# Kernel optimization log

Measured on AMD Instinct MI355X. Metric: run time of the kernel, lower is better.

Reference implementation:

```python
import jax, jax.numpy as jnp
import numpy as np

N = 8192      # source grid points
M = 8192      # output grid points
NB = 16       # n_basis
WIDTH = 32    # int(n_basis * enhancement)
EPS = 1e-4
LOG2 = 0.6931471805599453


def log_cosh(x):
    a = jnp.abs(x)
    return a + jnp.log1p(jnp.exp(-2.0 * a)) - LOG2


def setup_inputs() -> dict:
    key = jax.random.key(0)
    ks = jax.random.split(key, 9)
    rho = jax.random.uniform(ks[0], (N,), minval=0.05, maxval=2.0)
    gamma = jax.random.uniform(ks[1], (N,), minval=0.01, maxval=1.0)
    coords = jax.random.normal(ks[2], (N, 3)) * 5.0
    weights = jax.random.uniform(ks[3], (N,), minval=0.0, maxval=0.1)
    out_coords = jax.random.normal(ks[4], (M, 3)) * 5.0
    # field_embed params: Linear(1 -> WIDTH), Linear(WIDTH -> NB)
    w1 = jax.random.normal(ks[5], (1, WIDTH)) * 1.0
    b1 = jax.random.normal(ks[6], (WIDTH,)) * 0.1
    w2 = jax.random.normal(ks[7], (WIDTH, NB)) / np.sqrt(WIDTH)
    b2 = jax.random.normal(ks[8], (NB,)) * 0.1
    return {"rho": rho, "gamma": gamma, "coords": coords, "weights": weights,
            "out_coords": out_coords, "w1": w1, "b1": b1, "w2": w2, "b2": b2}


def _field_embed(x, w1, b1, w2, b2):
    # x: (..., 1) -> (..., NB)
    return jnp.tanh(x @ w1 + b1) @ w2 + b2


def reference(rho, gamma, coords, weights, out_coords, w1, b1, w2, b2):
    # rescaled (reduced) density gradient s^2 = gamma / (4 (3 pi^2)^{2/3} rho^{8/3})
    s2 = gamma / (4.0 * (3.0 * jnp.pi ** 2) ** (2.0 / 3.0) * rho ** (8.0 / 3.0))
    x = jnp.log(s2 + EPS)[:, None]                     # (N, 1)
    exponent = log_cosh(_field_embed(x, w1, b1, w2, b2))  # (N, NB)
    heg_scale = log_cosh(_field_embed(jnp.zeros((1, 1), rho.dtype), w1, b1, w2, b2)) ** 1.5  # (1, NB)
    beta = jnp.pi * (rho[:, None] / 2.0) ** (2.0 / 3.0) * exponent  # (N, NB)
    wrho = weights * rho                                # (N,)

    # all-pairs squared distances (M, N), computed once
    d2 = (jnp.sum(out_coords ** 2, axis=1)[:, None]
          + jnp.sum(coords ** 2, axis=1)[None, :]
          - 2.0 * out_coords @ coords.T)
    d2 = jnp.maximum(d2, 0.0)

    # KeOps Genred: y[i, b] = sum_j exp(-beta[j, b] * d2[i, j]) * wrho[j]
    # scan over the (small, fixed) basis axis so only one (M, N) kernel slice lives at a time
    def body(carry, beta_b):                            # beta_b: (N,)
        yb = jnp.exp(-d2 * beta_b[None, :]) @ wrho      # (M,)
        return carry, yb

    _, ys = jax.lax.scan(body, 0, beta.T)               # (NB, M)
    return ys.T * heg_scale                             # (M, NB)
```

## Files before the change

### kernel.cpp

```cpp
#include <hip/hip_runtime.h>
#include <hip/hip_bf16.h>


#define N_PTS 8192
#define M_PTS 8192
#define NBASIS 16
#define WIDTH 32

__device__ __forceinline__ float exp2_hw(float x) { return __builtin_amdgcn_exp2f(x); }
__device__ __forceinline__ float log2_hw(float x) { return __builtin_amdgcn_logf(x); }

__device__ __forceinline__ float fast_tanh(float z) {
    float a = fabsf(z);
    float t = __expf(-2.0f * a);
    float r = (1.0f - t) / (1.0f + t);
    return copysignf(r, z);
}

__device__ __forceinline__ float log_cosh_f(float x) {
    float a = fabsf(x);
    return a + __logf(1.0f + __expf(-2.0f * a)) - 0.6931471805599453f;
}

__global__ __launch_bounds__(256)
void cg_prep(const float* __restrict__ rho,
             const float* __restrict__ gamma,
             const float* __restrict__ coords,
             const float* __restrict__ weights,
             const float* __restrict__ w1,
             const float* __restrict__ b1,
             const float* __restrict__ w2,
             const float* __restrict__ b2,
             float4* __restrict__ cw,
             float4* __restrict__ bnq,
             float* __restrict__ hegf)
{
    const float PI_F = 3.14159265358979323846f;
    const float LOG2E = 1.4426950408889634f;

    __shared__ float s_w1[WIDTH], s_b1[WIDTH], s_w2[WIDTH * NBASIS], s_b2[NBASIS];
    int t = threadIdx.x;
    if (t < WIDTH) { s_w1[t] = w1[t]; s_b1[t] = b1[t]; }
    if (t < NBASIS) s_b2[t] = b2[t];
    s_w2[t] = w2[t];
    s_w2[t + 256] = w2[t + 256];
    __syncthreads();

    int j = blockIdx.x * blockDim.x + t;
    if (j < N_PTS) {
        float r = rho[j];
        float g = gamma[j];
        const float c83 = 38.28312007948569f;
        float r83 = exp2_hw(2.6666666667f * log2_hw(r));
        float s2 = g / (c83 * r83);
        float x = __logf(s2 + 1e-4f);

        float emb[NBASIS];
        #pragma unroll
        for (int b = 0; b < NBASIS; ++b) emb[b] = s_b2[b];
        #pragma unroll 4
        for (int w = 0; w < WIDTH; ++w) {
            float h = fast_tanh(fmaf(x, s_w1[w], s_b1[w]));
            #pragma unroll
            for (int b = 0; b < NBASIS; ++b)
                emb[b] = fmaf(h, s_w2[w * NBASIS + b], emb[b]);
        }
        float pref = PI_F * exp2_hw(0.6666666667f * log2_hw(0.5f * r));
        float scale = -LOG2E * pref;
        #pragma unroll
        for (int q = 0; q < 4; ++q) {
            bnq[q * N_PTS + j] = make_float4(scale * log_cosh_f(emb[4 * q + 0]),
                                             scale * log_cosh_f(emb[4 * q + 1]),
                                             scale * log_cosh_f(emb[4 * q + 2]),
                                             scale * log_cosh_f(emb[4 * q + 3]));
        }

        cw[j] = make_float4(coords[j * 3 + 0],
                            coords[j * 3 + 1],
                            coords[j * 3 + 2],
                            weights[j] * r);
    }

    if (blockIdx.x == 0 && t == 0) {
        float emb0[NBASIS];
        #pragma unroll
        for (int b = 0; b < NBASIS; ++b) emb0[b] = s_b2[b];
        for (int w = 0; w < WIDTH; ++w) {
            float h = fast_tanh(s_b1[w]);
            #pragma unroll
            for (int b = 0; b < NBASIS; ++b)
                emb0[b] = fmaf(h, s_w2[w * NBASIS + b], emb0[b]);
        }
        #pragma unroll
        for (int b = 0; b < NBASIS; ++b) {
            float lc = fmaxf(log_cosh_f(emb0[b]), 0.0f);
            hegf[b] = lc * sqrtf(lc);
        }
    }
}

__global__ __launch_bounds__(256, 4)
void cg_pairs(const float* __restrict__ oc,
              const float4* __restrict__ cw,
              const float4* __restrict__ bnq,
              const float* __restrict__ hegf,
              float* __restrict__ out)
{
    int wave = (blockIdx.x << 2) | (threadIdx.x >> 6);
    int lane = threadIdx.x & 63;
    int i0 = wave << 1;
    int i1 = i0 | 1;

    float ox0 = oc[i0 * 3 + 0], oy0 = oc[i0 * 3 + 1], oz0 = oc[i0 * 3 + 2];
    float ox1 = oc[i1 * 3 + 0], oy1 = oc[i1 * 3 + 1], oz1 = oc[i1 * 3 + 2];

    float acc0[NBASIS], acc1[NBASIS];
    #pragma unroll
    for (int b = 0; b < NBASIS; ++b) { acc0[b] = 0.0f; acc1[b] = 0.0f; }

    #pragma unroll 2
    for (int k = 0; k < N_PTS / 64; ++k) {
        int j = (k << 6) | lane;
        float4 c = cw[j];
        float dx0 = ox0 - c.x, dy0 = oy0 - c.y, dz0 = oz0 - c.z;
        float dx1 = ox1 - c.x, dy1 = oy1 - c.y, dz1 = oz1 - c.z;
        float d20 = fmaf(dx0, dx0, fmaf(dy0, dy0, dz0 * dz0));
        float d21 = fmaf(dx1, dx1, fmaf(dy1, dy1, dz1 * dz1));
        #pragma unroll
        for (int q = 0; q < 4; ++q) {
            float4 b4 = bnq[q * N_PTS + j];
            float e00 = exp2_hw(b4.x * d20);
            float e01 = exp2_hw(b4.y * d20);
            float e02 = exp2_hw(b4.z * d20);
            float e03 = exp2_hw(b4.w * d20);
            float e10 = exp2_hw(b4.x * d21);
            float e11 = exp2_hw(b4.y * d21);
            float e12 = exp2_hw(b4.z * d21);
            float e13 = exp2_hw(b4.w * d21);
            acc0[q * 4 + 0] = fmaf(e00, c.w, acc0[q * 4 + 0]);
            acc0[q * 4 + 1] = fmaf(e01, c.w, acc0[q * 4 + 1]);
            acc0[q * 4 + 2] = fmaf(e02, c.w, acc0[q * 4 + 2]);
            acc0[q * 4 + 3] = fmaf(e03, c.w, acc0[q * 4 + 3]);
            acc1[q * 4 + 0] = fmaf(e10, c.w, acc1[q * 4 + 0]);
            acc1[q * 4 + 1] = fmaf(e11, c.w, acc1[q * 4 + 1]);
            acc1[q * 4 + 2] = fmaf(e12, c.w, acc1[q * 4 + 2]);
            acc1[q * 4 + 3] = fmaf(e13, c.w, acc1[q * 4 + 3]);
        }
    }

    #pragma unroll
    for (int m = 1; m < 64; m <<= 1) {
        #pragma unroll
        for (int b = 0; b < NBASIS; ++b) {
            acc0[b] += __shfl_xor(acc0[b], m, 64);
            acc1[b] += __shfl_xor(acc1[b], m, 64);
        }
    }

    if (lane == 0) {
        const float4* hg = (const float4*)hegf;
        float4* o0 = (float4*)&out[i0 * NBASIS];
        float4* o1 = (float4*)&out[i1 * NBASIS];
        #pragma unroll
        for (int q = 0; q < 4; ++q) {
            float4 h = hg[q];
            o0[q] = make_float4(acc0[q * 4 + 0] * h.x, acc0[q * 4 + 1] * h.y,
                                acc0[q * 4 + 2] * h.z, acc0[q * 4 + 3] * h.w);
            o1[q] = make_float4(acc1[q * 4 + 0] * h.x, acc1[q * 4 + 1] * h.y,
                                acc1[q * 4 + 2] * h.z, acc1[q * 4 + 3] * h.w);
        }
    }
}

extern "C" void kernel_launch(void* const* d_in, const int* in_sizes, int n_in,
                              void* d_out, int out_size, void* d_ws, size_t ws_size,
                              hipStream_t stream) {
    const float* rho        = (const float*)d_in[0];
    const float* gamma      = (const float*)d_in[1];
    const float* coords     = (const float*)d_in[2];
    const float* weights    = (const float*)d_in[3];
    const float* out_coords = (const float*)d_in[4];
    const float* w1         = (const float*)d_in[5];
    const float* b1         = (const float*)d_in[6];
    const float* w2         = (const float*)d_in[7];
    const float* b2         = (const float*)d_in[8];

    char* ws = (char*)d_ws;
    float4* cw   = (float4*)(ws);
    float4* bnq  = (float4*)(ws + (128 << 10));
    float*  hegf = (float*) (ws + (640 << 10));

    cg_prep<<<N_PTS / 256, 256, 0, stream>>>(rho, gamma, coords, weights,
                                             w1, b1, w2, b2,
                                             cw, bnq, hegf);

    cg_pairs<<<M_PTS / 8, 256, 0, stream>>>(out_coords, cw, bnq, hegf,
                                            (float*)d_out);
}
```

Before: 208.6 us.

## Split source range across two waves with atomic output accumulation

The pairs kernel now assigns each pair of output points to two waves, each covering half of the source points, and combines the halves with atomicAdd into an output zeroed by a memset. This doubles the number of waves to raise occupancy and hide latency across the GPU. The prep kernel moves to 64-thread blocks so more blocks are spread across CUs. The cost is an extra memset launch, atomic traffic, and nondeterministic summation order.

New measurement: 235.0 us. 1.13x slower.

```diff
diff --git a/kernel.cpp b/kernel.cpp
--- a/kernel.cpp
+++ b/kernel.cpp
@@ -22,7 +22,7 @@
     return a + __logf(1.0f + __expf(-2.0f * a)) - 0.6931471805599453f;
 }
 
-__global__ __launch_bounds__(256)
+__global__ __launch_bounds__(64)
 void cg_prep(const float* __restrict__ rho,
              const float* __restrict__ gamma,
              const float* __restrict__ coords,
@@ -42,12 +42,12 @@
     int t = threadIdx.x;
     if (t < WIDTH) { s_w1[t] = w1[t]; s_b1[t] = b1[t]; }
     if (t < NBASIS) s_b2[t] = b2[t];
-    s_w2[t] = w2[t];
-    s_w2[t + 256] = w2[t + 256];
+    #pragma unroll
+    for (int k = 0; k < 8; ++k) s_w2[t + 64 * k] = w2[t + 64 * k];
     __syncthreads();
 
-    int j = blockIdx.x * blockDim.x + t;
-    if (j < N_PTS) {
+    int j = blockIdx.x * 64 + t;
+    {
         float r = rho[j];
         float g = gamma[j];
         const float c83 = 38.28312007948569f;
@@ -106,10 +106,13 @@
               const float* __restrict__ hegf,
               float* __restrict__ out)
 {
-    int wave = (blockIdx.x << 2) | (threadIdx.x >> 6);
+    int wid  = (blockIdx.x << 2) | (threadIdx.x >> 6);
     int lane = threadIdx.x & 63;
-    int i0 = wave << 1;
+    int pair = wid >> 1;
+    int half = wid & 1;
+    int i0 = pair << 1;
     int i1 = i0 | 1;
+    int jbase = half << 12;
 
     float ox0 = oc[i0 * 3 + 0], oy0 = oc[i0 * 3 + 1], oz0 = oc[i0 * 3 + 2];
     float ox1 = oc[i1 * 3 + 0], oy1 = oc[i1 * 3 + 1], oz1 = oc[i1 * 3 + 2];
@@ -119,8 +122,8 @@
     for (int b = 0; b < NBASIS; ++b) { acc0[b] = 0.0f; acc1[b] = 0.0f; }
 
     #pragma unroll 2
-    for (int k = 0; k < N_PTS / 64; ++k) {
-        int j = (k << 6) | lane;
+    for (int k = 0; k < 64; ++k) {
+        int j = jbase + (k << 6) + lane;
         float4 c = cw[j];
         float dx0 = ox0 - c.x, dy0 = oy0 - c.y, dz0 = oz0 - c.z;
         float dx1 = ox1 - c.x, dy1 = oy1 - c.y, dz1 = oz1 - c.z;
@@ -158,16 +161,11 @@
     }
 
     if (lane == 0) {
-        const float4* hg = (const float4*)hegf;
-        float4* o0 = (float4*)&out[i0 * NBASIS];
-        float4* o1 = (float4*)&out[i1 * NBASIS];
         #pragma unroll
-        for (int q = 0; q < 4; ++q) {
-            float4 h = hg[q];
-            o0[q] = make_float4(acc0[q * 4 + 0] * h.x, acc0[q * 4 + 1] * h.y,
-                                acc0[q * 4 + 2] * h.z, acc0[q * 4 + 3] * h.w);
-            o1[q] = make_float4(acc1[q * 4 + 0] * h.x, acc1[q * 4 + 1] * h.y,
-                                acc1[q * 4 + 2] * h.z, acc1[q * 4 + 3] * h.w);
+        for (int b = 0; b < NBASIS; ++b) {
+            float h = hegf[b];
+            atomicAdd(&out[i0 * NBASIS + b], acc0[b] * h);
+            atomicAdd(&out[i1 * NBASIS + b], acc1[b] * h);
         }
     }
 }
@@ -190,10 +188,12 @@
     float4* bnq  = (float4*)(ws + (128 << 10));
     float*  hegf = (float*) (ws + (640 << 10));
 
-    cg_prep<<<N_PTS / 256, 256, 0, stream>>>(rho, gamma, coords, weights,
-                                             w1, b1, w2, b2,
-                                             cw, bnq, hegf);
+    (void)hipMemsetAsync(d_out, 0, (size_t)M_PTS * NBASIS * sizeof(float), stream);
 
-    cg_pairs<<<M_PTS / 8, 256, 0, stream>>>(out_coords, cw, bnq, hegf,
+    cg_prep<<<N_PTS / 64, 64, 0, stream>>>(rho, gamma, coords, weights,
+                                           w1, b1, w2, b2,
+                                           cw, bnq, hegf);
+
+    cg_pairs<<<M_PTS / 4, 256, 0, stream>>>(out_coords, cw, bnq, hegf,
                                             (float*)d_out);
 }
```
